# Optimization experiments

Measured on AMD Instinct MI355X. Metric: run time of the kernel, lower is better.

## Reference

```python
import jax, jax.numpy as jnp
import numpy as np

N = 50000        # nodes
E = 800000       # edges (before self-loops)
NODE_IN = 128    # input feature dim
HID = 32         # per-head hidden dim
EPS = 1e-5       # batchnorm eps
NEG_SLOPE = 0.2  # GAT leaky-relu slope


def gat(x, src, dst, W, a_src, a_dst, b, heads, out_dim):
    """PyG-style GATConv (concat=True, self-loops added, eval-mode dropout)."""
    n = x.shape[0]
    h = (x @ W).reshape(n, heads, out_dim)                     # [n,H,D]
    loops = jnp.arange(n, dtype=src.dtype)
    s = jnp.concatenate([src, loops])                          # add self loops
    d = jnp.concatenate([dst, loops])
    e_src = jnp.einsum('nhd,hd->nh', h, a_src)                 # [n,H]
    e_dst = jnp.einsum('nhd,hd->nh', h, a_dst)
    alpha = jax.nn.leaky_relu(e_src[s] + e_dst[d], NEG_SLOPE)  # [E+n,H]
    m = jax.ops.segment_max(alpha, d, num_segments=n)          # segment softmax
    ex = jnp.exp(alpha - m[d])
    den = jax.ops.segment_sum(ex, d, num_segments=n)
    w = ex / den[d]                                            # [E+n,H]
    out = jax.ops.segment_sum(w[:, :, None] * h[s], d, num_segments=n)  # [n,H,D]
    return out.reshape(n, heads * out_dim) + b


def bn(x, gamma, beta):
    mu = x.mean(axis=0)
    var = x.var(axis=0)
    return (x - mu) * jax.lax.rsqrt(var + EPS) * gamma + beta


def setup_inputs() -> dict:
    key = jax.random.key(0)
    ks = jax.random.split(key, 20)
    nrm = lambda k, shape: jax.random.normal(k, shape, dtype=jnp.float32) * 0.1
    inp = {}
    inp['x'] = jax.random.normal(ks[0], (N, NODE_IN), dtype=jnp.float32)
    inp['edge_index'] = jax.random.randint(ks[1], (2, E), 0, N)
    inp['W1'] = nrm(ks[2], (NODE_IN, 4 * HID)); inp['as1'] = nrm(ks[3], (4, HID)); inp['ad1'] = nrm(ks[4], (4, HID)); inp['b1'] = jnp.zeros((4 * HID,))
    inp['g1'] = jnp.ones((4 * HID,)); inp['be1'] = jnp.zeros((4 * HID,))
    inp['W2'] = nrm(ks[5], (4 * HID, 4 * HID)); inp['as2'] = nrm(ks[6], (4, HID)); inp['ad2'] = nrm(ks[7], (4, HID)); inp['b2'] = jnp.zeros((4 * HID,))
    inp['g2'] = jnp.ones((4 * HID,)); inp['be2'] = jnp.zeros((4 * HID,))
    # encoder GAT3 (bottleneck): 128 -> 32, 1 head
    inp['W3'] = nrm(ks[8], (4 * HID, HID)); inp['as3'] = nrm(ks[9], (1, HID)); inp['ad3'] = nrm(ks[10], (1, HID)); inp['b3'] = jnp.zeros((HID,))
    # decoder GAT4: 32 -> 32, 1 head
    inp['W4'] = nrm(ks[11], (HID, HID)); inp['as4'] = nrm(ks[12], (1, HID)); inp['ad4'] = nrm(ks[13], (1, HID)); inp['b4'] = jnp.zeros((HID,))
    inp['g4'] = jnp.ones((HID,)); inp['be4'] = jnp.zeros((HID,))
    # decoder GAT5: 32 -> 128, 1 head
    inp['W5'] = nrm(ks[14], (HID, NODE_IN)); inp['as5'] = nrm(ks[15], (1, NODE_IN)); inp['ad5'] = nrm(ks[16], (1, NODE_IN)); inp['b5'] = jnp.zeros((NODE_IN,))
    return inp


def reference(x, edge_index, W1, as1, ad1, b1, g1, be1, W2, as2, ad2, b2, g2, be2,
              W3, as3, ad3, b3, W4, as4, ad4, b4, g4, be4, W5, as5, ad5, b5):
    src, dst = edge_index[0], edge_index[1]
    # encoder (dropout is identity in eval mode)
    h = jax.nn.relu(gat(x, src, dst, W1, as1, ad1, b1, heads=4, out_dim=HID))
    h = bn(h, g1, be1)
    h = jax.nn.relu(gat(h, src, dst, W2, as2, ad2, b2, heads=4, out_dim=HID))
    h = bn(h, g2, be2)
    h = jax.nn.relu(gat(h, src, dst, W3, as3, ad3, b3, heads=1, out_dim=HID))
    # decoder
    r = jax.nn.relu(gat(h, src, dst, W4, as4, ad4, b4, heads=1, out_dim=HID))
    r = jax.nn.relu(bn(r, g4, be4))
    return gat(r, src, dst, W5, as5, ad5, b5, heads=1, out_dim=NODE_IN)
```

## Files before the change

kernel.cpp:

```cpp
#include <hip/hip_runtime.h>
#include <math.h>

#define NNODES 50000
#define NEDGES 800000
#define BN_EPS 1e-5f
#define DEGC 128
#define NB 391
#define NPB 128
#define SCG 256
#define HWG 192
#define NSH 32

typedef unsigned int uint;
typedef unsigned short ushort;
typedef __attribute__((ext_vector_type(8))) short bf16x8;
typedef __attribute__((ext_vector_type(4))) float f32x4;

static __device__ __forceinline__ ushort f2bf(float f) {
    uint u = __float_as_uint(f);
    return (ushort)((u + 0x7fffu + ((u >> 16) & 1u)) >> 16);
}
static __device__ __forceinline__ float bfhi(ushort h) {
    return __uint_as_float((uint)h << 16);
}
static __device__ __forceinline__ float2 bf2f(uint v) {
    float2 r;
    r.x = __uint_as_float(v << 16);
    r.y = __uint_as_float(v & 0xffff0000u);
    return r;
}
static __device__ __forceinline__ void splitbf(float v, ushort& h, ushort& l) {
    h = f2bf(v);
    l = f2bf(v - bfhi(h));
}

__global__ __launch_bounds__(256) void histwt(const int* __restrict__ dst,
                                              int* __restrict__ bcnt,
                                              const float* __restrict__ W1,
                                              const float* __restrict__ W2,
                                              const float* __restrict__ W3,
                                              ushort* __restrict__ wt1h, ushort* __restrict__ wt1l,
                                              ushort* __restrict__ wt2h, ushort* __restrict__ wt2l,
                                              ushort* __restrict__ wt3h, ushort* __restrict__ wt3l) {
    if (blockIdx.x < HWG) {
        __shared__ int h[NB];
        for (int i = threadIdx.x; i < NB; i += 256) h[i] = 0;
        __syncthreads();
        for (int e = blockIdx.x * 256 + threadIdx.x; e < NEDGES; e += HWG * 256)
            atomicAdd(&h[dst[e] >> 7], 1);
        __syncthreads();
        for (int i = threadIdx.x; i < NB; i += 256)
            if (h[i]) atomicAdd(&bcnt[i], h[i]);
    } else {
        int idx = (blockIdx.x - HWG) * 256 + threadIdx.x;
        ushort h, l;
        if (idx < 16384) {
            int k = idx >> 7, c = idx & 127;
            splitbf(W1[idx], h, l);
            wt1h[c * 128 + k] = h; wt1l[c * 128 + k] = l;
        } else if (idx < 32768) {
            int i = idx - 16384;
            int k = i >> 7, c = i & 127;
            splitbf(W2[i], h, l);
            wt2h[c * 128 + k] = h; wt2l[c * 128 + k] = l;
        } else {
            int i = idx - 32768;
            int k = i >> 5, c = i & 31;
            splitbf(W3[i], h, l);
            wt3h[c * 128 + k] = h; wt3l[c * 128 + k] = l;
        }
    }
}

__global__ void bucket_scan(const int* __restrict__ bcnt, int* __restrict__ eoff,
                            int* __restrict__ boff, int* __restrict__ ecur,
                            int* __restrict__ off, const float* __restrict__ W5,
                            const float* __restrict__ as5, const float* __restrict__ ad5,
                            float* __restrict__ atl) {
    __shared__ int w1[8], w2[8];
    int t = threadIdx.x, lane = t & 63, wv = t >> 6;
    int v = (t < NB) ? bcnt[t] : 0;
    int nib = 0;
    if (t < NB) nib = (t == NB - 1) ? (NNODES - (NB - 1) * NPB) : NPB;
    int x1 = v, x2 = v + nib;
#pragma unroll
    for (int s = 1; s < 64; s <<= 1) {
        int t1 = __shfl_up(x1, s), t2 = __shfl_up(x2, s);
        if (lane >= s) { x1 += t1; x2 += t2; }
    }
    if (lane == 63) { w1[wv] = x1; w2[wv] = x2; }
    __syncthreads();
    if (wv == 0) {
        int a = (lane < 8) ? w1[lane] : 0, b = (lane < 8) ? w2[lane] : 0;
#pragma unroll
        for (int s = 1; s < 8; s <<= 1) {
            int ta = __shfl_up(a, s), tb = __shfl_up(b, s);
            if (lane >= s) { a += ta; b += tb; }
        }
        if (lane < 8) { w1[lane] = a; w2[lane] = b; }
    }
    __syncthreads();
    int p1 = (wv > 0) ? w1[wv - 1] : 0, p2 = (wv > 0) ? w2[wv - 1] : 0;
    x1 += p1; x2 += p2;
    if (t < NB) { eoff[t] = x1 - v; boff[t] = x2 - (v + nib); ecur[t] = 0; }
    if (t == NB - 1) { eoff[NB] = x1; boff[NB] = x2; off[NNODES] = x2; }
    if (t >= 448) {
        int idx = t - 448;
        int k = idx & 31;
        const float* a = (idx < 32) ? as5 : ad5;
        float s = 0.f;
        for (int f = 0; f < 128; ++f) s += W5[k * 128 + f] * a[f];
        atl[idx] = s;
    }
}

__global__ __launch_bounds__(256) void scatter_mm(const int* __restrict__ src,
                                                  const int* __restrict__ dst,
                                                  const int* __restrict__ eoff,
                                                  int* __restrict__ ecur,
                                                  uint* __restrict__ ebuf,
                                                  const float* __restrict__ X,
                                                  const ushort* __restrict__ Wth,
                                                  const ushort* __restrict__ Wtl,
                                                  const float* __restrict__ av_s,
                                                  const float* __restrict__ av_d,
                                                  ushort* __restrict__ Obf,
                                                  float* __restrict__ es,
                                                  float* __restrict__ ed, int N) {
    __shared__ int lh[NB];
    __shared__ int lcur[NB];
    __shared__ __align__(16) ushort sAh[64 * 136];
    __shared__ __align__(16) ushort sAl[64 * 136];
    int tid = threadIdx.x;
    if (blockIdx.x < SCG) {
        const int CH = (NEDGES + SCG - 1) / SCG;
        int c0 = blockIdx.x * CH;
        int c1 = min(c0 + CH, NEDGES);
        for (int i = tid; i < NB; i += 256) { lh[i] = 0; lcur[i] = 0; }
        __syncthreads();
        for (int e = c0 + tid; e < c1; e += 256) atomicAdd(&lh[dst[e] >> 7], 1);
        __syncthreads();
        for (int i = tid; i < NB; i += 256) {
            int c = lh[i];
            lh[i] = c ? (eoff[i] + atomicAdd(&ecur[i], c)) : 0;
        }
        __syncthreads();
        for (int e = c0 + tid; e < c1; e += 256) {
            int d = dst[e];
            int bk = d >> 7;
            int p = lh[bk] + atomicAdd(&lcur[bk], 1);
            ebuf[p] = ((uint)(d & 127) << 16) | (uint)src[e];
        }
        return;
    }
    int rowBase = (int)(blockIdx.x - SCG) * 64;
    int lane = tid & 63, wv = tid >> 6;
    int lr = lane & 15, lq = lane >> 4;
#pragma unroll
    for (int j = 0; j < 8; ++j) {
        int idx = tid + j * 256;
        int row = idx >> 5;
        int cq = idx & 31;
        int gr = rowBase + row;
        float4 v = make_float4(0.f, 0.f, 0.f, 0.f);
        if (gr < N) v = *(const float4*)(X + (size_t)gr * 128 + cq * 4);
        ushort h0, h1, h2, h3, l0, l1, l2, l3;
        splitbf(v.x, h0, l0); splitbf(v.y, h1, l1);
        splitbf(v.z, h2, l2); splitbf(v.w, h3, l3);
        uint2 ph, pl;
        ph.x = (uint)h0 | ((uint)h1 << 16);
        ph.y = (uint)h2 | ((uint)h3 << 16);
        pl.x = (uint)l0 | ((uint)l1 << 16);
        pl.y = (uint)l2 | ((uint)l3 << 16);
        *(uint2*)&sAh[row * 136 + cq * 4] = ph;
        *(uint2*)&sAl[row * 136 + cq * 4] = pl;
    }
    __syncthreads();
    const int ncol0 = wv * 32;
    f32x4 acc[4][2];
#pragma unroll
    for (int mi = 0; mi < 4; ++mi)
#pragma unroll
        for (int ni = 0; ni < 2; ++ni) acc[mi][ni] = (f32x4){0.f, 0.f, 0.f, 0.f};
#pragma unroll
    for (int kq = 0; kq < 4; ++kq) {
        int kb = kq * 32 + lq * 8;
        bf16x8 ah[4], al[4], bh[2], bl[2];
#pragma unroll
        for (int mi = 0; mi < 4; ++mi) {
            ah[mi] = *(const bf16x8*)&sAh[(16 * mi + lr) * 136 + kb];
            al[mi] = *(const bf16x8*)&sAl[(16 * mi + lr) * 136 + kb];
        }
#pragma unroll
        for (int ni = 0; ni < 2; ++ni) {
            size_t bo = (size_t)(ncol0 + 16 * ni + lr) * 128 + kb;
            bh[ni] = *(const bf16x8*)(Wth + bo);
            bl[ni] = *(const bf16x8*)(Wtl + bo);
        }
#pragma unroll
        for (int mi = 0; mi < 4; ++mi)
#pragma unroll
            for (int ni = 0; ni < 2; ++ni) {
                acc[mi][ni] = __builtin_amdgcn_mfma_f32_16x16x32_bf16(
                    ah[mi], bh[ni], acc[mi][ni], 0, 0, 0);
                acc[mi][ni] = __builtin_amdgcn_mfma_f32_16x16x32_bf16(
                    al[mi], bh[ni], acc[mi][ni], 0, 0, 0);
                acc[mi][ni] = __builtin_amdgcn_mfma_f32_16x16x32_bf16(
                    ah[mi], bl[ni], acc[mi][ni], 0, 0, 0);
            }
    }
    {
        float as0 = av_s[ncol0 + lr], as1 = av_s[ncol0 + 16 + lr];
        float ad0 = av_d[ncol0 + lr], ad1 = av_d[ncol0 + 16 + lr];
#pragma unroll
        for (int mi = 0; mi < 4; ++mi)
#pragma unroll
            for (int r = 0; r < 4; ++r) {
                float ps = acc[mi][0][r] * as0 + acc[mi][1][r] * as1;
                float pd = acc[mi][0][r] * ad0 + acc[mi][1][r] * ad1;
#pragma unroll
                for (int s = 1; s < 16; s <<= 1) {
                    ps += __shfl_xor(ps, s);
                    pd += __shfl_xor(pd, s);
                }
                if (lr == 0) {
                    int gr = rowBase + 16 * mi + lq * 4 + r;
                    if (gr < N) {
                        es[(size_t)gr * 4 + wv] = ps;
                        ed[(size_t)gr * 4 + wv] = pd;
                    }
                }
            }
    }
    __syncthreads();
#pragma unroll
    for (int mi = 0; mi < 4; ++mi)
#pragma unroll
        for (int ni = 0; ni < 2; ++ni)
#pragma unroll
            for (int r = 0; r < 4; ++r)
                sAh[(16 * mi + lq * 4 + r) * 136 + ncol0 + 16 * ni + lr] =
                    f2bf(acc[mi][ni][r]);
    __syncthreads();
    int row = tid >> 2, c0 = (tid & 3) * 32;
    int gr = rowBase + row;
    if (gr < N) {
        uint4 o0 = *(const uint4*)&sAh[row * 136 + c0];
        uint4 o1 = *(const uint4*)&sAh[row * 136 + c0 + 8];
        uint4 o2 = *(const uint4*)&sAh[row * 136 + c0 + 16];
        uint4 o3 = *(const uint4*)&sAh[row * 136 + c0 + 24];
        uint4* d4 = (uint4*)(Obf + (size_t)gr * 128 + c0);
        d4[0] = o0; d4[1] = o1; d4[2] = o2; d4[3] = o3;
    }
}

__global__ __launch_bounds__(256) void bucket_place(const uint* __restrict__ ebuf,
                                                    const int* __restrict__ eoff,
                                                    const int* __restrict__ boff,
                                                    int* __restrict__ off,
                                                    int* __restrict__ ssorted) {
    __shared__ int cnt[NPB];
    __shared__ int cur[NPB];
    __shared__ int wtot[2];
    int b = blockIdx.x;
    int nib = (b == NB - 1) ? (NNODES - (NB - 1) * NPB) : NPB;
    int t = threadIdx.x;
    for (int i = t; i < NPB; i += 256) { cnt[i] = 0; cur[i] = 0; }
    __syncthreads();
    int e0 = eoff[b], e1 = eoff[b + 1];
    for (int i = e0 + t; i < e1; i += 256) atomicAdd(&cnt[ebuf[i] >> 16], 1);
    __syncthreads();
    int lane = t & 63, wv = t >> 6;
    int deg = (t < nib) ? cnt[t] + 1 : 0;
    int x = deg;
#pragma unroll
    for (int s = 1; s < 64; s <<= 1) {
        int tv = __shfl_up(x, s);
        if (lane >= s) x += tv;
    }
    if (lane == 63 && wv < 2) wtot[wv] = x;
    __syncthreads();
    int excl = x - deg + ((wv == 1) ? wtot[0] : 0);
    if (t < nib) {
        int base = boff[b] + excl;
        off[b * NPB + t] = base;
        cnt[t] = excl;
        ssorted[base + deg - 1] = b * NPB + t;
    }
    __syncthreads();
    int bb = boff[b];
    for (int i = e0 + t; i < e1; i += 256) {
        uint v = ebuf[i];
        int ld = v >> 16;
        int pos = bb + cnt[ld] + atomicAdd(&cur[ld], 1);
        ssorted[pos] = (int)(v & 0xffffu);
    }
}

template <int KK, bool WBF, bool AFF>
__global__ __launch_bounds__(256) void mfma_mm(const float* __restrict__ X,
                                               const ushort* __restrict__ Wth,
                                               const ushort* __restrict__ Wtl,
                                               const float* __restrict__ bnsums,
                                               const float* __restrict__ bng,
                                               const float* __restrict__ bnbe,
                                               const float* __restrict__ av_s,
                                               const float* __restrict__ av_d,
                                               float* __restrict__ Of,
                                               ushort* __restrict__ Obf,
                                               float* __restrict__ es,
                                               float* __restrict__ ed,
                                               int N, float inv_n) {
    constexpr int KQ = KK / 32;
    constexpr int MI = WBF ? 4 : 1;
    __shared__ __align__(16) ushort sAh[64 * 136];
    __shared__ __align__(16) ushort sAl[64 * 136];
    __shared__ float sSc[128], sSh[128];
    int tid = threadIdx.x;
    int rowBase = blockIdx.x * 64;
    int lane = tid & 63, wv = tid >> 6;
    int lr = lane & 15, lq = lane >> 4;

    if constexpr (AFF) {
        if (tid < KK) {
            float su = 0.f, sq = 0.f;
#pragma unroll 4
            for (int sh = 0; sh < NSH; ++sh) {
                su += bnsums[sh * 256 + tid];
                sq += bnsums[sh * 256 + 128 + tid];
            }
            float mu = su * inv_n;
            float var = sq * inv_n - mu * mu;
            float s = bng[tid] * rsqrtf(var + BN_EPS);
            sSc[tid] = s;
            sSh[tid] = fmaf(-mu, s, bnbe[tid]);
        }
        __syncthreads();
    }

#pragma unroll
    for (int j = 0; j < 64 * KK / 4 / 256; ++j) {
        int idx = tid + j * 256;
        int row = idx / (KK / 4);
        int cq = idx - row * (KK / 4);
        int gr = rowBase + row;
        float4 v = make_float4(0.f, 0.f, 0.f, 0.f);
        if (gr < N) {
            v = *(const float4*)(X + (size_t)gr * KK + cq * 4);
            if constexpr (AFF) {
                int c = cq * 4;
                v.x = fmaf(v.x, sSc[c], sSh[c]);
                v.y = fmaf(v.y, sSc[c + 1], sSh[c + 1]);
                v.z = fmaf(v.z, sSc[c + 2], sSh[c + 2]);
                v.w = fmaf(v.w, sSc[c + 3], sSh[c + 3]);
            }
        }
        ushort h0, h1, h2, h3, l0, l1, l2, l3;
        splitbf(v.x, h0, l0); splitbf(v.y, h1, l1);
        splitbf(v.z, h2, l2); splitbf(v.w, h3, l3);
        uint2 ph, pl;
        ph.x = (uint)h0 | ((uint)h1 << 16);
        ph.y = (uint)h2 | ((uint)h3 << 16);
        pl.x = (uint)l0 | ((uint)l1 << 16);
        pl.y = (uint)l2 | ((uint)l3 << 16);
        *(uint2*)&sAh[row * 136 + cq * 4] = ph;
        *(uint2*)&sAl[row * 136 + cq * 4] = pl;
    }
    __syncthreads();

    const int mrow0 = WBF ? 0 : wv * 16;
    const int ncol0 = WBF ? wv * 32 : 0;
    f32x4 acc[MI][2];
#pragma unroll
    for (int mi = 0; mi < MI; ++mi)
#pragma unroll
        for (int ni = 0; ni < 2; ++ni) acc[mi][ni] = (f32x4){0.f, 0.f, 0.f, 0.f};

#pragma unroll
    for (int kq = 0; kq < KQ; ++kq) {
        int kb = kq * 32 + lq * 8;
        bf16x8 ah[MI], al[MI], bh[2], bl[2];
#pragma unroll
        for (int mi = 0; mi < MI; ++mi) {
            ah[mi] = *(const bf16x8*)&sAh[(mrow0 + 16 * mi + lr) * 136 + kb];
            al[mi] = *(const bf16x8*)&sAl[(mrow0 + 16 * mi + lr) * 136 + kb];
        }
#pragma unroll
        for (int ni = 0; ni < 2; ++ni) {
            size_t bo = (size_t)(ncol0 + 16 * ni + lr) * KK + kb;
            bh[ni] = *(const bf16x8*)(Wth + bo);
            bl[ni] = *(const bf16x8*)(Wtl + bo);
        }
#pragma unroll
        for (int mi = 0; mi < MI; ++mi)
#pragma unroll
            for (int ni = 0; ni < 2; ++ni) {
                acc[mi][ni] = __builtin_amdgcn_mfma_f32_16x16x32_bf16(
                    ah[mi], bh[ni], acc[mi][ni], 0, 0, 0);
                acc[mi][ni] = __builtin_amdgcn_mfma_f32_16x16x32_bf16(
                    al[mi], bh[ni], acc[mi][ni], 0, 0, 0);
                acc[mi][ni] = __builtin_amdgcn_mfma_f32_16x16x32_bf16(
                    ah[mi], bl[ni], acc[mi][ni], 0, 0, 0);
            }
    }

    {
        float as0 = av_s[ncol0 + lr], as1 = av_s[ncol0 + 16 + lr];
        float ad0 = av_d[ncol0 + lr], ad1 = av_d[ncol0 + 16 + lr];
#pragma unroll
        for (int mi = 0; mi < MI; ++mi)
#pragma unroll
            for (int r = 0; r < 4; ++r) {
                float ps = acc[mi][0][r] * as0 + acc[mi][1][r] * as1;
                float pd = acc[mi][0][r] * ad0 + acc[mi][1][r] * ad1;
#pragma unroll
                for (int s = 1; s < 16; s <<= 1) {
                    ps += __shfl_xor(ps, s);
                    pd += __shfl_xor(pd, s);
                }
                if (lr == 0) {
                    int gr = rowBase + mrow0 + 16 * mi + lq * 4 + r;
                    if (gr < N) {
                        if constexpr (WBF) {
                            es[(size_t)gr * 4 + wv] = ps;
                            ed[(size_t)gr * 4 + wv] = pd;
                        } else {
                            es[gr] = ps;
                            ed[gr] = pd;
                        }
                    }
                }
            }
    }
    __syncthreads();

    if constexpr (WBF) {
#pragma unroll
        for (int mi = 0; mi < MI; ++mi)
#pragma unroll
            for (int ni = 0; ni < 2; ++ni)
#pragma unroll
                for (int r = 0; r < 4; ++r)
                    sAh[(16 * mi + lq * 4 + r) * 136 + ncol0 + 16 * ni + lr] =
                        f2bf(acc[mi][ni][r]);
        __syncthreads();
        int row = tid >> 2, c0 = (tid & 3) * 32;
        int gr = rowBase + row;
        if (gr < N) {
            uint4 o0 = *(const uint4*)&sAh[row * 136 + c0];
            uint4 o1 = *(const uint4*)&sAh[row * 136 + c0 + 8];
            uint4 o2 = *(const uint4*)&sAh[row * 136 + c0 + 16];
            uint4 o3 = *(const uint4*)&sAh[row * 136 + c0 + 24];
            uint4* d4 = (uint4*)(Obf + (size_t)gr * 128 + c0);
            d4[0] = o0; d4[1] = o1; d4[2] = o2; d4[3] = o3;
        }
    } else {
        float* sOutF = (float*)sAh;
#pragma unroll
        for (int ni = 0; ni < 2; ++ni)
#pragma unroll
            for (int r = 0; r < 4; ++r)
                sOutF[(mrow0 + lq * 4 + r) * 36 + 16 * ni + lr] = acc[0][ni][r];
        __syncthreads();
        int row = tid >> 2, c0 = (tid & 3) * 8;
        int gr = rowBase + row;
        if (gr < N) {
            float4 v0 = *(const float4*)&sOutF[row * 36 + c0];
            float4 v1 = *(const float4*)&sOutF[row * 36 + c0 + 4];
            *(float4*)(Of + (size_t)gr * 32 + c0) = v0;
            *(float4*)(Of + (size_t)gr * 32 + c0 + 4) = v1;
        }
    }
}

__global__ __launch_bounds__(256) void node_agg_bf4(const int* __restrict__ off,
                                                    const int* __restrict__ ssorted,
                                                    const ushort* __restrict__ Hb,
                                                    const float* __restrict__ es,
                                                    const float* __restrict__ ed,
                                                    const float* __restrict__ bias,
                                                    float* __restrict__ outp,
                                                    float* __restrict__ sums) {
    __shared__ float lds_ex[4][DEGC * 4];
    __shared__ int lds_s[4][DEGC];
    __shared__ float red_v[4][128];
    __shared__ float red_q[4][128];
    int wib = threadIdx.x >> 6;
    int lane = threadIdx.x & 63;
    int d = blockIdx.x * 4 + wib;
    int beg = off[d], end = off[d + 1];
    int m = end - beg;

    int lh = lane & 3, le = lane >> 2;
    float edl = ed[(size_t)d * 4 + lh];
    float denp = 0.f;
    for (int base = 0; base < m; base += 16) {
        int e = base + le;
        if (e < m) {
            int s = ssorted[beg + e];
            if (lh == 0 && e < DEGC) lds_s[wib][e] = s;
            float a = es[(size_t)s * 4 + lh] + edl;
            a = a > 0.f ? a : 0.2f * a;
            float ex = __expf(a);
            denp += ex;
            if (e < DEGC) lds_ex[wib][e * 4 + lh] = ex;
        }
    }
#pragma unroll
    for (int sft = 4; sft < 64; sft <<= 1) denp += __shfl_xor(denp, sft);
    float inv = 1.f / denp;
    int mu = m < DEGC ? m : DEGC;
    for (int idx = lane; idx < mu * 4; idx += 64) lds_ex[wib][idx] *= inv;

    const uint* Hu = (const uint*)Hb;
    int head = lane >> 4;
    float inv2 = __shfl(inv, head);
    float edl2 = __shfl(edl, head);
    float acc0 = 0.f, acc1 = 0.f;
    int i = 0;
    for (; i + 8 <= mu; i += 8) {
        int sx[8];
        float wx[8];
        uint vx[8];
#pragma unroll
        for (int j = 0; j < 8; ++j) {
            sx[j] = lds_s[wib][i + j];
            wx[j] = lds_ex[wib][(i + j) * 4 + head];
        }
#pragma unroll
        for (int j = 0; j < 8; ++j) vx[j] = Hu[(size_t)sx[j] * 64 + lane];
#pragma unroll
        for (int j = 0; j < 8; ++j) {
            float2 f = bf2f(vx[j]);
            acc0 += wx[j] * f.x;
            acc1 += wx[j] * f.y;
        }
    }
    for (; i < mu; ++i) {
        int s = lds_s[wib][i];
        float w = lds_ex[wib][i * 4 + head];
        float2 f = bf2f(Hu[(size_t)s * 64 + lane]);
        acc0 += w * f.x;
        acc1 += w * f.y;
    }
    for (; i < m; ++i) {
        int s = ssorted[beg + i];
        float a = es[(size_t)s * 4 + head] + edl2;
        a = a > 0.f ? a : 0.2f * a;
        float w = __expf(a) * inv2;
        float2 f = bf2f(Hu[(size_t)s * 64 + lane]);
        acc0 += w * f.x;
        acc1 += w * f.y;
    }
    float v0 = fmaxf(acc0 + bias[2 * lane], 0.f);
    float v1 = fmaxf(acc1 + bias[2 * lane + 1], 0.f);
    *(float2*)(outp + (size_t)d * 128 + 2 * lane) = make_float2(v0, v1);

    red_v[wib][2 * lane] = v0;
    red_v[wib][2 * lane + 1] = v1;
    red_q[wib][2 * lane] = v0 * v0;
    red_q[wib][2 * lane + 1] = v1 * v1;
    __syncthreads();
    int t = threadIdx.x;
    int sh = (blockIdx.x & (NSH - 1)) * 256;
    if (t < 128) {
        float s = red_v[0][t] + red_v[1][t] + red_v[2][t] + red_v[3][t];
        atomicAdd(&sums[sh + t], s);
    } else {
        int u = t - 128;
        float q = red_q[0][u] + red_q[1][u] + red_q[2][u] + red_q[3][u];
        atomicAdd(&sums[sh + 128 + u], q);
    }
}

__global__ __launch_bounds__(256) void node_agg_f32s(const int* __restrict__ off,
                                                     const int* __restrict__ ssorted,
                                                     const float* __restrict__ Hb,
                                                     const float* __restrict__ es,
                                                     const float* __restrict__ ed,
                                                     const float* __restrict__ bias,
                                                     float* __restrict__ outp,
                                                     float* __restrict__ sums) {
    __shared__ float lds_ex[8][DEGC];
    __shared__ int lds_s[8][DEGC];
    __shared__ float red_v[8][32];
    __shared__ float red_q[8][32];
    int tid = threadIdx.x;
    int wib = tid >> 6, lane = tid & 63;
    int grp = lane >> 5, g = lane & 31;
    int nn = wib * 2 + grp;
    int d = blockIdx.x * 8 + nn;
    int beg = off[d], end = off[d + 1];
    int m = end - beg;

    float edv = ed[d];
    float denp = 0.f;
    for (int base = 0; base < m; base += 32) {
        int e = base + g;
        if (e < m) {
            int s = ssorted[beg + e];
            if (e < DEGC) lds_s[nn][e] = s;
            float a = es[s] + edv;
            a = a > 0.f ? a : 0.2f * a;
            float ex = __expf(a);
            denp += ex;
            if (e < DEGC) lds_ex[nn][e] = ex;
        }
    }
#pragma unroll
    for (int sft = 1; sft < 32; sft <<= 1) denp += __shfl_xor(denp, sft);
    int mu = m < DEGC ? m : DEGC;
    float inv = 1.f / denp;
    for (int idx = g; idx < mu; idx += 32) lds_ex[nn][idx] *= inv;

    int f = g;
    float acc = 0.f;
    int i = 0;
    for (; i + 8 <= mu; i += 8) {
        int sx[8];
        float wx[8], hx[8];
#pragma unroll
        for (int j = 0; j < 8; ++j) { sx[j] = lds_s[nn][i + j]; wx[j] = lds_ex[nn][i + j]; }
#pragma unroll
        for (int j = 0; j < 8; ++j) hx[j] = Hb[(size_t)sx[j] * 32 + f];
#pragma unroll
        for (int j = 0; j < 8; ++j) acc += wx[j] * hx[j];
    }
    for (; i < mu; ++i) {
        int s = lds_s[nn][i];
        acc += lds_ex[nn][i] * Hb[(size_t)s * 32 + f];
    }
    for (; i < m; ++i) {
        int s = ssorted[beg + i];
        float a = es[s] + edv;
        a = a > 0.f ? a : 0.2f * a;
        acc += __expf(a) * inv * Hb[(size_t)s * 32 + f];
    }
    float v = fmaxf(acc + bias[f], 0.f);
    outp[(size_t)d * 32 + f] = v;
    red_v[nn][f] = v;
    red_q[nn][f] = v * v;
    __syncthreads();
    int sh = (blockIdx.x & (NSH - 1)) * 64;
    if (tid < 32) {
        float s = 0.f;
#pragma unroll
        for (int k = 0; k < 8; ++k) s += red_v[k][tid];
        atomicAdd(&sums[sh + tid], s);
    } else if (tid < 64) {
        int u = tid - 32;
        float q = 0.f;
#pragma unroll
        for (int k = 0; k < 8; ++k) q += red_q[k][u];
        atomicAdd(&sums[sh + 32 + u], q);
    }
}

__global__ __launch_bounds__(256) void agg_mm32(const int* __restrict__ off,
                                                const int* __restrict__ ssorted,
                                                const float* __restrict__ Hb,
                                                const float* __restrict__ es,
                                                const float* __restrict__ ed,
                                                const float* __restrict__ bias,
                                                const float* __restrict__ W4,
                                                const float* __restrict__ as4,
                                                const float* __restrict__ ad4,
                                                float* __restrict__ outp,
                                                float* __restrict__ es_o,
                                                float* __restrict__ ed_o) {
    __shared__ float lds_ex[8][DEGC];
    __shared__ int lds_s[8][DEGC];
    __shared__ float sW[32][32];
    __shared__ float sV[8][32];
    int tid = threadIdx.x;
    for (int i = tid; i < 1024; i += 256) sW[i >> 5][i & 31] = W4[i];
    __syncthreads();
    int wib = tid >> 6, lane = tid & 63;
    int grp = lane >> 5, g = lane & 31;
    int nn = wib * 2 + grp;
    int d = blockIdx.x * 8 + nn;
    int beg = off[d], end = off[d + 1];
    int m = end - beg;

    float edv = ed[d];
    float denp = 0.f;
    for (int base = 0; base < m; base += 32) {
        int e = base + g;
        if (e < m) {
            int s = ssorted[beg + e];
            if (e < DEGC) lds_s[nn][e] = s;
            float a = es[s] + edv;
            a = a > 0.f ? a : 0.2f * a;
            float ex = __expf(a);
            denp += ex;
            if (e < DEGC) lds_ex[nn][e] = ex;
        }
    }
#pragma unroll
    for (int sft = 1; sft < 32; sft <<= 1) denp += __shfl_xor(denp, sft);
    int mu = m < DEGC ? m : DEGC;
    float inv = 1.f / denp;
    for (int idx = g; idx < mu; idx += 32) lds_ex[nn][idx] *= inv;

    int f = g;
    float acc = 0.f;
    int i = 0;
    for (; i + 8 <= mu; i += 8) {
        int sx[8];
        float wx[8], hx[8];
#pragma unroll
        for (int j = 0; j < 8; ++j) { sx[j] = lds_s[nn][i + j]; wx[j] = lds_ex[nn][i + j]; }
#pragma unroll
        for (int j = 0; j < 8; ++j) hx[j] = Hb[(size_t)sx[j] * 32 + f];
#pragma unroll
        for (int j = 0; j < 8; ++j) acc += wx[j] * hx[j];
    }
    for (; i < mu; ++i) {
        int s = lds_s[nn][i];
        acc += lds_ex[nn][i] * Hb[(size_t)s * 32 + f];
    }
    for (; i < m; ++i) {
        int s = ssorted[beg + i];
        float a = es[s] + edv;
        a = a > 0.f ? a : 0.2f * a;
        acc += __expf(a) * inv * Hb[(size_t)s * 32 + f];
    }
    float v = fmaxf(acc + bias[f], 0.f);
    sV[nn][f] = v;
    float o = 0.f;
#pragma unroll
    for (int f2 = 0; f2 < 32; ++f2) o = fmaf(sV[nn][f2], sW[f2][f], o);
    outp[(size_t)d * 32 + f] = o;
    float ps = o * as4[f], pd = o * ad4[f];
#pragma unroll
    for (int sft = 1; sft < 32; sft <<= 1) { ps += __shfl_xor(ps, sft); pd += __shfl_xor(pd, sft); }
    if (g == 0) { es_o[d] = ps; ed_o[d] = pd; }
}

__global__ __launch_bounds__(256) void agg_mm128(const int* __restrict__ off,
                                                 const int* __restrict__ ssorted,
                                                 const float* __restrict__ Hb,
                                                 const float* __restrict__ es,
                                                 const float* __restrict__ ed,
                                                 const float* __restrict__ W5,
                                                 const float* __restrict__ b5,
                                                 float* __restrict__ outp) {
    __shared__ float lds_ex[8][DEGC];
    __shared__ int lds_s[8][DEGC];
    __shared__ float sW[32][128];
    __shared__ float sV[8][32];
    int tid = threadIdx.x;
    for (int i = tid; i < 4096; i += 256) ((float*)sW)[i] = W5[i];
    __syncthreads();
    int wib = tid >> 6, lane = tid & 63;
    int grp = lane >> 5, g = lane & 31;
    int nn = wib * 2 + grp;
    int d = blockIdx.x * 8 + nn;
    int beg = off[d], end = off[d + 1];
    int m = end - beg;

    float edv = ed[d];
    float denp = 0.f;
    for (int base = 0; base < m; base += 32) {
        int e = base + g;
        if (e < m) {
            int s = ssorted[beg + e];
            if (e < DEGC) lds_s[nn][e] = s;
            float a = es[s] + edv;
            a = a > 0.f ? a : 0.2f * a;
            float ex = __expf(a);
            denp += ex;
            if (e < DEGC) lds_ex[nn][e] = ex;
        }
    }
#pragma unroll
    for (int sft = 1; sft < 32; sft <<= 1) denp += __shfl_xor(denp, sft);
    int mu = m < DEGC ? m : DEGC;
    float inv = 1.f / denp;
    for (int idx = g; idx < mu; idx += 32) lds_ex[nn][idx] *= inv;

    int f = g;
    float acc = 0.f;
    int i = 0;
    for (; i + 8 <= mu; i += 8) {
        int sx[8];
        float wx[8], hx[8];
#pragma unroll
        for (int j = 0; j < 8; ++j) { sx[j] = lds_s[nn][i + j]; wx[j] = lds_ex[nn][i + j]; }
#pragma unroll
        for (int j = 0; j < 8; ++j) hx[j] = Hb[(size_t)sx[j] * 32 + f];
#pragma unroll
        for (int j = 0; j < 8; ++j) acc += wx[j] * hx[j];
    }
    for (; i < mu; ++i) {
        int s = lds_s[nn][i];
        acc += lds_ex[nn][i] * Hb[(size_t)s * 32 + f];
    }
    for (; i < m; ++i) {
        int s = ssorted[beg + i];
        float a = es[s] + edv;
        a = a > 0.f ? a : 0.2f * a;
        acc += __expf(a) * inv * Hb[(size_t)s * 32 + f];
    }
    sV[nn][f] = acc;
    float o0 = 0.f, o1 = 0.f, o2 = 0.f, o3 = 0.f;
    int c = g * 4;
#pragma unroll
    for (int f2 = 0; f2 < 32; ++f2) {
        float vv = sV[nn][f2];
        float4 w4 = *(const float4*)&sW[f2][c];
        o0 = fmaf(vv, w4.x, o0);
        o1 = fmaf(vv, w4.y, o1);
        o2 = fmaf(vv, w4.z, o2);
        o3 = fmaf(vv, w4.w, o3);
    }
    float4 rb = *(const float4*)&b5[c];
    *(float4*)(outp + (size_t)d * 128 + c) =
        make_float4(o0 + rb.x, o1 + rb.y, o2 + rb.z, o3 + rb.w);
}

__global__ __launch_bounds__(256) void bn_relu_attn(const float* __restrict__ y,
                                                    const float* __restrict__ sums,
                                                    const float* __restrict__ g,
                                                    const float* __restrict__ be,
                                                    const float* __restrict__ atl,
                                                    float* __restrict__ o,
                                                    float* __restrict__ es,
                                                    float* __restrict__ ed) {
    __shared__ float ssc[32], ssh[32];
    int t = threadIdx.x;
    if (t < 32) {
        float su = 0.f, sq = 0.f;
#pragma unroll 4
        for (int sh = 0; sh < NSH; ++sh) { su += sums[sh * 64 + t]; sq += sums[sh * 64 + 32 + t]; }
        float mu = su / (float)NNODES;
        float var = sq / (float)NNODES - mu * mu;
        float sc = rsqrtf(var + BN_EPS) * g[t];
        ssc[t] = sc;
        ssh[t] = fmaf(-mu, sc, be[t]);
    }
    __syncthreads();
    int r = blockIdx.x * 8 + (t >> 5);
    int f = t & 31;
    float v = fmaxf(fmaf(y[(size_t)r * 32 + f], ssc[f], ssh[f]), 0.f);
    o[(size_t)r * 32 + f] = v;
    float ps = v * atl[f], pd = v * atl[32 + f];
#pragma unroll
    for (int s = 1; s < 32; s <<= 1) { ps += __shfl_xor(ps, s); pd += __shfl_xor(pd, s); }
    if (f == 0) { es[r] = ps; ed[r] = pd; }
}

extern "C" void kernel_launch(void* const* d_in, const int* in_sizes, int n_in, void* d_out,
                              int out_size, void* d_ws, size_t ws_size, hipStream_t stream) {
    const int N = NNODES, E = NEDGES;
    const float* x = (const float*)d_in[0];
    const int* ei = (const int*)d_in[1];
    const int* src = ei;
    const int* dst = ei + E;
    const float* W1 = (const float*)d_in[2];
    const float* as1 = (const float*)d_in[3];
    const float* ad1 = (const float*)d_in[4];
    const float* b1 = (const float*)d_in[5];
    const float* g1 = (const float*)d_in[6];
    const float* be1 = (const float*)d_in[7];
    const float* W2 = (const float*)d_in[8];
    const float* as2 = (const float*)d_in[9];
    const float* ad2 = (const float*)d_in[10];
    const float* b2 = (const float*)d_in[11];
    const float* g2 = (const float*)d_in[12];
    const float* be2 = (const float*)d_in[13];
    const float* W3 = (const float*)d_in[14];
    const float* as3 = (const float*)d_in[15];
    const float* ad3 = (const float*)d_in[16];
    const float* b3 = (const float*)d_in[17];
    const float* W4 = (const float*)d_in[18];
    const float* as4 = (const float*)d_in[19];
    const float* ad4 = (const float*)d_in[20];
    const float* b4 = (const float*)d_in[21];
    const float* g4 = (const float*)d_in[22];
    const float* be4 = (const float*)d_in[23];
    const float* W5 = (const float*)d_in[24];
    const float* as5 = (const float*)d_in[25];
    const float* ad5 = (const float*)d_in[26];
    const float* b5 = (const float*)d_in[27];
    float* out = (float*)d_out;

    float* ws = (float*)d_ws;
    float* bufAf = ws;
    float* bufB = ws + (size_t)N * 128;
    ushort* bufAbf = (ushort*)(ws + (size_t)2 * N * 128);
    uint* ebuf = (uint*)bufAf;
    float* esA = ws + (size_t)2 * N * 128 + (size_t)N * 64;
    float* edA = esA + (size_t)N * 4;
    float* esB = edA + (size_t)N * 4;
    float* edB = esB + (size_t)N * 4;
    float* sums = edB + (size_t)N * 4;
    float* sumsA = sums;
    float* sumsB = sums + (size_t)NSH * 256;
    float* sums32 = sums + (size_t)2 * NSH * 256;
    int* bcnt = (int*)(sums + (size_t)NSH * 576);
    int* eoff = bcnt + NB;
    int* boff = eoff + NB + 1;
    int* ecur = boff + NB + 1;
    float* atl = (float*)(ecur + NB);
    int* off = (int*)(atl + 64);
    int* ssorted = off + N + 1;
    size_t wtoff = (((size_t)((ssorted + E + N) - (int*)ws)) + 3) & ~(size_t)3;
    ushort* wt1h = (ushort*)((int*)ws + wtoff);
    ushort* wt1l = wt1h + 16384;
    ushort* wt2h = wt1l + 16384;
    ushort* wt2l = wt2h + 16384;
    ushort* wt3h = wt2l + 16384;
    ushort* wt3l = wt3h + 4096;

    const int TB = 256;
    const int gAgg = N / 4;
    const int gAgg2 = N / 8;
    const int gMM = (N + 63) / 64;
    const float inv_n = 1.f / (float)N;

    hipMemsetAsync(sums, 0, ((size_t)NSH * 576 + NB) * sizeof(float), stream);

    histwt<<<HWG + 144, TB, 0, stream>>>(dst, bcnt, W1, W2, W3, wt1h, wt1l, wt2h, wt2l,
                                         wt3h, wt3l);
    bucket_scan<<<1, 512, 0, stream>>>(bcnt, eoff, boff, ecur, off, W5, as5, ad5, atl);

    scatter_mm<<<SCG + gMM, TB, 0, stream>>>(src, dst, eoff, ecur, ebuf, x, wt1h, wt1l,
                                             as1, ad1, bufAbf, esA, edA, N);
    bucket_place<<<NB, TB, 0, stream>>>(ebuf, eoff, boff, off, ssorted);

    node_agg_bf4<<<gAgg, TB, 0, stream>>>(off, ssorted, bufAbf, esA, edA, b1, bufB, sumsA);

    mfma_mm<128, true, true><<<gMM, TB, 0, stream>>>(
        bufB, wt2h, wt2l, sumsA, g1, be1, as2, ad2, nullptr, bufAbf, esB, edB,
        N, inv_n);
    node_agg_bf4<<<gAgg, TB, 0, stream>>>(off, ssorted, bufAbf, esB, edB, b2, bufB, sumsB);

    mfma_mm<128, false, true><<<gMM, TB, 0, stream>>>(
        bufB, wt3h, wt3l, sumsB, g2, be2, as3, ad3, bufAf, nullptr, esA, edA,
        N, inv_n);

    agg_mm32<<<gAgg2, TB, 0, stream>>>(off, ssorted, bufAf, esA, edA, b3, W4, as4, ad4,
                                       bufB, esB, edB);

    node_agg_f32s<<<gAgg2, TB, 0, stream>>>(off, ssorted, bufB, esB, edB, b4, bufAf, sums32);
    bn_relu_attn<<<N / 8, TB, 0, stream>>>(bufAf, sums32, g4, be4, atl, bufB, esA, edA);

    agg_mm128<<<gAgg2, TB, 0, stream>>>(off, ssorted, bufB, esA, edA, W5, b5, out);
}
```

Measured before the change: 412.8 us.

## Fuse softmax denominator into single-pass edge aggregation, drop LDS staging

All four node aggregation kernels now compute the attention exponentials, the softmax denominator and the weighted feature sum in a single pass over each node's edges. Normalisation happens once at the end by multiplying by the reciprocal of the denominator. This removes the first pass that gathered source indices and exponentials into shared memory, the cross-lane reduction, and the shared-memory staging, which also frees LDS for occupancy. In exchange, each lane recomputes the exp for its head or feature redundantly, re-reads the source index and es values per lane, and skips max-subtraction as before.

```diff
diff --git a/kernel.cpp b/kernel.cpp
--- a/kernel.cpp
+++ b/kernel.cpp
@@ -4,7 +4,6 @@
 #define NNODES 50000
 #define NEDGES 800000
 #define BN_EPS 1e-5f
-#define DEGC 128
 #define NB 391
 #define NPB 128
 #define SCG 256
@@ -481,8 +480,6 @@
                                                     const float* __restrict__ bias,
                                                     float* __restrict__ outp,
                                                     float* __restrict__ sums) {
-    __shared__ float lds_ex[4][DEGC * 4];
-    __shared__ int lds_s[4][DEGC];
     __shared__ float red_v[4][128];
     __shared__ float red_q[4][128];
     int wib = threadIdx.x >> 6;
@@ -490,70 +487,46 @@
     int d = blockIdx.x * 4 + wib;
     int beg = off[d], end = off[d + 1];
     int m = end - beg;
-
-    int lh = lane & 3, le = lane >> 2;
-    float edl = ed[(size_t)d * 4 + lh];
-    float denp = 0.f;
-    for (int base = 0; base < m; base += 16) {
-        int e = base + le;
-        if (e < m) {
-            int s = ssorted[beg + e];
-            if (lh == 0 && e < DEGC) lds_s[wib][e] = s;
-            float a = es[(size_t)s * 4 + lh] + edl;
+    int head = lane >> 4;
+    float edl = ed[(size_t)d * 4 + head];
+    const uint* Hu = (const uint*)Hb;
+    float den = 0.f, acc0 = 0.f, acc1 = 0.f;
+    int i = 0;
+    for (; i + 8 <= m; i += 8) {
+        int sx[8];
+        float ev[8];
+        uint vx[8];
+#pragma unroll
+        for (int j = 0; j < 8; ++j) sx[j] = ssorted[beg + i + j];
+#pragma unroll
+        for (int j = 0; j < 8; ++j) {
+            ev[j] = es[(size_t)sx[j] * 4 + head];
+            vx[j] = Hu[(size_t)sx[j] * 64 + lane];
+        }
+#pragma unroll
+        for (int j = 0; j < 8; ++j) {
+            float a = ev[j] + edl;
             a = a > 0.f ? a : 0.2f * a;
             float ex = __expf(a);
-            denp += ex;
-            if (e < DEGC) lds_ex[wib][e * 4 + lh] = ex;
-        }
-    }
-#pragma unroll
-    for (int sft = 4; sft < 64; sft <<= 1) denp += __shfl_xor(denp, sft);
-    float inv = 1.f / denp;
-    int mu = m < DEGC ? m : DEGC;
-    for (int idx = lane; idx < mu * 4; idx += 64) lds_ex[wib][idx] *= inv;
-
-    const uint* Hu = (const uint*)Hb;
-    int head = lane >> 4;
-    float inv2 = __shfl(inv, head);
-    float edl2 = __shfl(edl, head);
-    float acc0 = 0.f, acc1 = 0.f;
-    int i = 0;
-    for (; i + 8 <= mu; i += 8) {
-        int sx[8];
-        float wx[8];
-        uint vx[8];
-#pragma unroll
-        for (int j = 0; j < 8; ++j) {
-            sx[j] = lds_s[wib][i + j];
-            wx[j] = lds_ex[wib][(i + j) * 4 + head];
-        }
-#pragma unroll
-        for (int j = 0; j < 8; ++j) vx[j] = Hu[(size_t)sx[j] * 64 + lane];
-#pragma unroll
-        for (int j = 0; j < 8; ++j) {
+            den += ex;
             float2 f = bf2f(vx[j]);
-            acc0 += wx[j] * f.x;
-            acc1 += wx[j] * f.y;
-        }
-    }
-    for (; i < mu; ++i) {
-        int s = lds_s[wib][i];
-        float w = lds_ex[wib][i * 4 + head];
-        float2 f = bf2f(Hu[(size_t)s * 64 + lane]);
-        acc0 += w * f.x;
-        acc1 += w * f.y;
+            acc0 += ex * f.x;
+            acc1 += ex * f.y;
+        }
     }
     for (; i < m; ++i) {
         int s = ssorted[beg + i];
-        float a = es[(size_t)s * 4 + head] + edl2;
+        float a = es[(size_t)s * 4 + head] + edl;
         a = a > 0.f ? a : 0.2f * a;
-        float w = __expf(a) * inv2;
+        float ex = __expf(a);
+        den += ex;
         float2 f = bf2f(Hu[(size_t)s * 64 + lane]);
-        acc0 += w * f.x;
-        acc1 += w * f.y;
-    }
-    float v0 = fmaxf(acc0 + bias[2 * lane], 0.f);
-    float v1 = fmaxf(acc1 + bias[2 * lane + 1], 0.f);
+        acc0 += ex * f.x;
+        acc1 += ex * f.y;
+    }
+    float inv = 1.f / den;
+    float v0 = fmaxf(fmaf(acc0, inv, bias[2 * lane]), 0.f);
+    float v1 = fmaxf(fmaf(acc1, inv, bias[2 * lane + 1]), 0.f);
     *(float2*)(outp + (size_t)d * 128 + 2 * lane) = make_float2(v0, v1);
 
     red_v[wib][2 * lane] = v0;
@@ -581,8 +554,6 @@
                                                      const float* __restrict__ bias,
                                                      float* __restrict__ outp,
                                                      float* __restrict__ sums) {
-    __shared__ float lds_ex[8][DEGC];
-    __shared__ int lds_s[8][DEGC];
     __shared__ float red_v[8][32];
     __shared__ float red_q[8][32];
     int tid = threadIdx.x;
@@ -594,52 +565,40 @@
     int m = end - beg;
 
     float edv = ed[d];
-    float denp = 0.f;
-    for (int base = 0; base < m; base += 32) {
-        int e = base + g;
-        if (e < m) {
-            int s = ssorted[beg + e];
-            if (e < DEGC) lds_s[nn][e] = s;
-            float a = es[s] + edv;
+    float den = 0.f, acc = 0.f;
+    int i = 0;
+    for (; i + 8 <= m; i += 8) {
+        int sx[8];
+        float ev[8], hx[8];
+#pragma unroll
+        for (int j = 0; j < 8; ++j) sx[j] = ssorted[beg + i + j];
+#pragma unroll
+        for (int j = 0; j < 8; ++j) {
+            ev[j] = es[sx[j]];
+            hx[j] = Hb[(size_t)sx[j] * 32 + g];
+        }
+#pragma unroll
+        for (int j = 0; j < 8; ++j) {
+            float a = ev[j] + edv;
             a = a > 0.f ? a : 0.2f * a;
             float ex = __expf(a);
-            denp += ex;
-            if (e < DEGC) lds_ex[nn][e] = ex;
-        }
-    }
-#pragma unroll
-    for (int sft = 1; sft < 32; sft <<= 1) denp += __shfl_xor(denp, sft);
-    int mu = m < DEGC ? m : DEGC;
-    float inv = 1.f / denp;
-    for (int idx = g; idx < mu; idx += 32) lds_ex[nn][idx] *= inv;
-
-    int f = g;
-    float acc = 0.f;
-    int i = 0;
-    for (; i + 8 <= mu; i += 8) {
-        int sx[8];
-        float wx[8], hx[8];
-#pragma unroll
-        for (int j = 0; j < 8; ++j) { sx[j] = lds_s[nn][i + j]; wx[j] = lds_ex[nn][i + j]; }
-#pragma unroll
-        for (int j = 0; j < 8; ++j) hx[j] = Hb[(size_t)sx[j] * 32 + f];
-#pragma unroll
-        for (int j = 0; j < 8; ++j) acc += wx[j] * hx[j];
-    }
-    for (; i < mu; ++i) {
-        int s = lds_s[nn][i];
-        acc += lds_ex[nn][i] * Hb[(size_t)s * 32 + f];
+            den += ex;
+            acc += ex * hx[j];
+        }
     }
     for (; i < m; ++i) {
         int s = ssorted[beg + i];
         float a = es[s] + edv;
         a = a > 0.f ? a : 0.2f * a;
-        acc += __expf(a) * inv * Hb[(size_t)s * 32 + f];
-    }
-    float v = fmaxf(acc + bias[f], 0.f);
-    outp[(size_t)d * 32 + f] = v;
-    red_v[nn][f] = v;
-    red_q[nn][f] = v * v;
+        float ex = __expf(a);
+        den += ex;
+        acc += ex * Hb[(size_t)s * 32 + g];
+    }
+    float inv = 1.f / den;
+    float v = fmaxf(fmaf(acc, inv, bias[g]), 0.f);
+    outp[(size_t)d * 32 + g] = v;
+    red_v[nn][g] = v;
+    red_q[nn][g] = v * v;
     __syncthreads();
     int sh = (blockIdx.x & (NSH - 1)) * 64;
     if (tid < 32) {
@@ -668,8 +627,6 @@
                                                 float* __restrict__ outp,
                                                 float* __restrict__ es_o,
                                                 float* __restrict__ ed_o) {
-    __shared__ float lds_ex[8][DEGC];
-    __shared__ int lds_s[8][DEGC];
     __shared__ float sW[32][32];
     __shared__ float sV[8][32];
     int tid = threadIdx.x;
@@ -683,55 +640,43 @@
     int m = end - beg;
 
     float edv = ed[d];
-    float denp = 0.f;
-    for (int base = 0; base < m; base += 32) {
-        int e = base + g;
-        if (e < m) {
-            int s = ssorted[beg + e];
-            if (e < DEGC) lds_s[nn][e] = s;
-            float a = es[s] + edv;
+    float den = 0.f, acc = 0.f;
+    int i = 0;
+    for (; i + 8 <= m; i += 8) {
+        int sx[8];
+        float ev[8], hx[8];
+#pragma unroll
+        for (int j = 0; j < 8; ++j) sx[j] = ssorted[beg + i + j];
+#pragma unroll
+        for (int j = 0; j < 8; ++j) {
+            ev[j] = es[sx[j]];
+            hx[j] = Hb[(size_t)sx[j] * 32 + g];
+        }
+#pragma unroll
+        for (int j = 0; j < 8; ++j) {
+            float a = ev[j] + edv;
             a = a > 0.f ? a : 0.2f * a;
             float ex = __expf(a);
-            denp += ex;
-            if (e < DEGC) lds_ex[nn][e] = ex;
-        }
-    }
-#pragma unroll
-    for (int sft = 1; sft < 32; sft <<= 1) denp += __shfl_xor(denp, sft);
-    int mu = m < DEGC ? m : DEGC;
-    float inv = 1.f / denp;
-    for (int idx = g; idx < mu; idx += 32) lds_ex[nn][idx] *= inv;
-
-    int f = g;
-    float acc = 0.f;
-    int i = 0;
-    for (; i + 8 <= mu; i += 8) {
-        int sx[8];
-        float wx[8], hx[8];
-#pragma unroll
-        for (int j = 0; j < 8; ++j) { sx[j] = lds_s[nn][i + j]; wx[j] = lds_ex[nn][i + j]; }
-#pragma unroll
-        for (int j = 0; j < 8; ++j) hx[j] = Hb[(size_t)sx[j] * 32 + f];
-#pragma unroll
-        for (int j = 0; j < 8; ++j) acc += wx[j] * hx[j];
-    }
-    for (; i < mu; ++i) {
-        int s = lds_s[nn][i];
-        acc += lds_ex[nn][i] * Hb[(size_t)s * 32 + f];
+            den += ex;
+            acc += ex * hx[j];
+        }
     }
     for (; i < m; ++i) {
         int s = ssorted[beg + i];
         float a = es[s] + edv;
         a = a > 0.f ? a : 0.2f * a;
-        acc += __expf(a) * inv * Hb[(size_t)s * 32 + f];
-    }
-    float v = fmaxf(acc + bias[f], 0.f);
-    sV[nn][f] = v;
+        float ex = __expf(a);
+        den += ex;
+        acc += ex * Hb[(size_t)s * 32 + g];
+    }
+    float inv = 1.f / den;
+    float v = fmaxf(fmaf(acc, inv, bias[g]), 0.f);
+    sV[nn][g] = v;
     float o = 0.f;
 #pragma unroll
-    for (int f2 = 0; f2 < 32; ++f2) o = fmaf(sV[nn][f2], sW[f2][f], o);
-    outp[(size_t)d * 32 + f] = o;
-    float ps = o * as4[f], pd = o * ad4[f];
+    for (int f2 = 0; f2 < 32; ++f2) o = fmaf(sV[nn][f2], sW[f2][g], o);
+    outp[(size_t)d * 32 + g] = o;
+    float ps = o * as4[g], pd = o * ad4[g];
 #pragma unroll
     for (int sft = 1; sft < 32; sft <<= 1) { ps += __shfl_xor(ps, sft); pd += __shfl_xor(pd, sft); }
     if (g == 0) { es_o[d] = ps; ed_o[d] = pd; }
@@ -745,8 +690,6 @@
                                                  const float* __restrict__ W5,
                                                  const float* __restrict__ b5,
                                                  float* __restrict__ outp) {
-    __shared__ float lds_ex[8][DEGC];
-    __shared__ int lds_s[8][DEGC];
     __shared__ float sW[32][128];
     __shared__ float sV[8][32];
     int tid = threadIdx.x;
@@ -760,49 +703,36 @@
     int m = end - beg;
 
     float edv = ed[d];
-    float denp = 0.f;
-    for (int base = 0; base < m; base += 32) {
-        int e = base + g;
-        if (e < m) {
-            int s = ssorted[beg + e];
-            if (e < DEGC) lds_s[nn][e] = s;
-            float a = es[s] + edv;
+    float den = 0.f, acc = 0.f;
+    int i = 0;
+    for (; i + 8 <= m; i += 8) {
+        int sx[8];
+        float ev[8], hx[8];
+#pragma unroll
+        for (int j = 0; j < 8; ++j) sx[j] = ssorted[beg + i + j];
+#pragma unroll
+        for (int j = 0; j < 8; ++j) {
+            ev[j] = es[sx[j]];
+            hx[j] = Hb[(size_t)sx[j] * 32 + g];
+        }
+#pragma unroll
+        for (int j = 0; j < 8; ++j) {
+            float a = ev[j] + edv;
             a = a > 0.f ? a : 0.2f * a;
             float ex = __expf(a);
-            denp += ex;
-            if (e < DEGC) lds_ex[nn][e] = ex;
-        }
-    }
-#pragma unroll
-    for (int sft = 1; sft < 32; sft <<= 1) denp += __shfl_xor(denp, sft);
-    int mu = m < DEGC ? m : DEGC;
-    float inv = 1.f / denp;
-    for (int idx = g; idx < mu; idx += 32) lds_ex[nn][idx] *= inv;
-
-    int f = g;
-    float acc = 0.f;
-    int i = 0;
-    for (; i + 8 <= mu; i += 8) {
-        int sx[8];
-        float wx[8], hx[8];
-#pragma unroll
-        for (int j = 0; j < 8; ++j) { sx[j] = lds_s[nn][i + j]; wx[j] = lds_ex[nn][i + j]; }
-#pragma unroll
-        for (int j = 0; j < 8; ++j) hx[j] = Hb[(size_t)sx[j] * 32 + f];
-#pragma unroll
-        for (int j = 0; j < 8; ++j) acc += wx[j] * hx[j];
-    }
-    for (; i < mu; ++i) {
-        int s = lds_s[nn][i];
-        acc += lds_ex[nn][i] * Hb[(size_t)s * 32 + f];
+            den += ex;
+            acc += ex * hx[j];
+        }
     }
     for (; i < m; ++i) {
         int s = ssorted[beg + i];
         float a = es[s] + edv;
         a = a > 0.f ? a : 0.2f * a;
-        acc += __expf(a) * inv * Hb[(size_t)s * 32 + f];
-    }
-    sV[nn][f] = acc;
+        float ex = __expf(a);
+        den += ex;
+        acc += ex * Hb[(size_t)s * 32 + g];
+    }
+    sV[nn][g] = acc * (1.f / den);
     float o0 = 0.f, o1 = 0.f, o2 = 0.f, o3 = 0.f;
     int c = g * 4;
 #pragma unroll
```

New measurement: 427.7 us. 3.6% more time.
